# Performance work log

Hardware: AMD Instinct MI355X
Metric: run time of the kernel (lower is better)

The kernel has to match this reference:

```python
import jax, jax.numpy as jnp
import numpy as np

N_NODES = 50000
N_EDGES = 800000
NUM_FEATURES = 128
HIDDEN = 128
NUM_CLASSES = 10
NUM_GRAPHS = 512
PROCESSING_STEPS = 4


def setup_inputs() -> dict:
    key = jax.random.key(0)
    ks = jax.random.split(key, 20)
    s = 0.05
    inp = {
        'x': jax.random.normal(ks[0], (N_NODES, NUM_FEATURES), jnp.float32),
        'edge_index': jax.random.randint(ks[1], (2, N_EDGES), 0, N_NODES),
        'batch': jnp.sort(jax.random.randint(ks[2], (N_NODES,), 0, NUM_GRAPHS)),
        # GCN layers (weights stored [in, out])
        'W1': jax.random.normal(ks[3], (NUM_FEATURES, HIDDEN), jnp.float32) * s,
        'b1': jnp.zeros((HIDDEN,), jnp.float32),
        'W2': jax.random.normal(ks[4], (HIDDEN, HIDDEN), jnp.float32) * s,
        'b2': jnp.zeros((HIDDEN,), jnp.float32),
        'W3': jax.random.normal(ks[5], (HIDDEN, HIDDEN), jnp.float32) * s,
        'b3': jnp.zeros((HIDDEN,), jnp.float32),
        # Set2Set LSTM cell: input 2*HIDDEN -> hidden HIDDEN, torch gate order i,f,g,o
        'Wih': jax.random.normal(ks[6], (4 * HIDDEN, 2 * HIDDEN), jnp.float32) * s,
        'Whh': jax.random.normal(ks[7], (4 * HIDDEN, HIDDEN), jnp.float32) * s,
        'bih': jnp.zeros((4 * HIDDEN,), jnp.float32),
        'bhh': jnp.zeros((4 * HIDDEN,), jnp.float32),
        # MLP head
        'L1w': jax.random.normal(ks[8], (2 * HIDDEN, HIDDEN), jnp.float32) * s,
        'L1b': jnp.zeros((HIDDEN,), jnp.float32),
        'L2w': jax.random.normal(ks[9], (HIDDEN, HIDDEN // 2), jnp.float32) * s,
        'L2b': jnp.zeros((HIDDEN // 2,), jnp.float32),
        'L3w': jax.random.normal(ks[10], (HIDDEN // 2, NUM_CLASSES), jnp.float32) * s,
        'L3b': jnp.zeros((NUM_CLASSES,), jnp.float32),
    }
    return inp


def _gcn_conv(x, row, col, W, b, n):
    # PyG GCNConv: x @ W, symmetric normalization with self-loops, scatter-add to targets.
    xw = x @ W  # [N, out]
    deg = jax.ops.segment_sum(jnp.ones_like(col, dtype=xw.dtype), col, num_segments=n)
    dis = jnp.where(deg > 0, jax.lax.rsqrt(jnp.maximum(deg, 1.0)), 0.0)
    norm = dis[row] * dis[col]  # [E+N]
    out = jax.ops.segment_sum(norm[:, None] * xw[row], col, num_segments=n)
    return out + b


def _segment_softmax(e, batch, n_seg):
    emax = jax.lax.stop_gradient(jax.ops.segment_max(e, batch, num_segments=n_seg))
    emax = jnp.where(jnp.isfinite(emax), emax, 0.0)
    a = jnp.exp(e - emax[batch])
    asum = jax.ops.segment_sum(a, batch, num_segments=n_seg)
    return a / jnp.where(asum > 0, asum, 1.0)[batch]


def reference(x, edge_index, batch, W1, b1, W2, b2, W3, b3,
              Wih, Whh, bih, bhh, L1w, L1b, L2w, L2b, L3w, L3b):
    n = x.shape[0]
    # add self loops once
    loops = jnp.arange(n, dtype=edge_index.dtype)
    row = jnp.concatenate([edge_index[0], loops])  # sources
    col = jnp.concatenate([edge_index[1], loops])  # targets

    h = jax.nn.relu(_gcn_conv(x, row, col, W1, b1, n))
    h = jax.nn.relu(_gcn_conv(h, row, col, W2, b2, n))
    h = jax.nn.relu(_gcn_conv(h, row, col, W3, b3, n))

    # Set2Set readout (processing_steps=4)
    d = h.shape[1]
    hs = jnp.zeros((NUM_GRAPHS, d), h.dtype)
    cs = jnp.zeros((NUM_GRAPHS, d), h.dtype)
    q_star = jnp.zeros((NUM_GRAPHS, 2 * d), h.dtype)
    for _ in range(PROCESSING_STEPS):
        gates = q_star @ Wih.T + hs @ Whh.T + bih + bhh  # [B, 4d]
        ig, fg, gg, og = jnp.split(gates, 4, axis=-1)
        cs = jax.nn.sigmoid(fg) * cs + jax.nn.sigmoid(ig) * jnp.tanh(gg)
        q = jax.nn.sigmoid(og) * jnp.tanh(cs)
        hs = q
        e = jnp.sum(h * q[batch], axis=-1)  # [N]
        a = _segment_softmax(e, batch, NUM_GRAPHS)
        r = jax.ops.segment_sum(a[:, None] * h, batch, num_segments=NUM_GRAPHS)
        q_star = jnp.concatenate([q, r], axis=-1)

    # MLP head (dropout inactive in eval)
    y = jax.nn.relu(q_star @ L1w + L1b)
    y = jax.nn.relu(y @ L2w + L2b)
    y = y @ L3w + L3b
    return jax.nn.log_softmax(y, axis=-1)
```

## Files before the change

### kernel.cpp

```cpp
#include <hip/hip_runtime.h>

constexpr int NN  = 50000;
constexpr int NE  = 800000;
constexpr int FD  = 128;
constexpr int NG  = 512;
constexpr int NB  = 4;
constexpr int BCAP = 24;
constexpr int CAP = NB * BCAP;
constexpr int SLICE = 12500;

typedef __attribute__((ext_vector_type(8))) short bf16x8;
typedef __attribute__((ext_vector_type(4))) float f32x4;

__device__ __forceinline__ float bf2f(unsigned short u) {
    unsigned int v = ((unsigned int)u) << 16;
    float f; __builtin_memcpy(&f, &v, 4); return f;
}
__device__ __forceinline__ unsigned short f2bf(float f) {
    unsigned int u; __builtin_memcpy(&u, &f, 4);
    u += 0x7FFFu + ((u >> 16) & 1u);
    return (unsigned short)(u >> 16);
}
__device__ __forceinline__ float2 bfp(unsigned int u) {
    unsigned int lo = u << 16, hi = u & 0xFFFF0000u;
    float2 r; __builtin_memcpy(&r.x, &lo, 4); __builtin_memcpy(&r.y, &hi, 4);
    return r;
}
__device__ __forceinline__ unsigned int packbf(float a, float b) {
    return (unsigned int)f2bf(a) | ((unsigned int)f2bf(b) << 16);
}
__device__ __forceinline__ float sigmoidf(float x) { return 1.0f / (1.0f + __expf(-x)); }
__device__ __forceinline__ float ldw(const void* p, int idx, int flag) {
    return flag ? ((const float*)p)[idx] : bf2f(((const unsigned short*)p)[idx]);
}

__global__ void k_detect(const unsigned int* __restrict__ xw, int* __restrict__ flag,
                         int* __restrict__ bcnt) {
    int gid = blockIdx.x * 256 + threadIdx.x;
    if (gid < NN * NB) bcnt[gid] = 0;
    if (blockIdx.x == 0) {
        __shared__ int cnt;
        if (threadIdx.x == 0) cnt = 0;
        __syncthreads();
        int local = 0;
        for (int i = threadIdx.x; i < 2048; i += 256) {
            unsigned int w = xw[i];
            unsigned int h0 = w & 0xFFFFu, h1 = w >> 16;
            if (((h0 >> 7) & 0xFF) >= 0x90) local++;
            if (((h1 >> 7) & 0xFF) >= 0x90) local++;
        }
        atomicAdd(&cnt, local);
        __syncthreads();
        if (threadIdx.x == 0) *flag = (cnt > 256) ? 1 : 0;
    }
}

__global__ void k_cvt_x(const void* __restrict__ src, unsigned short* __restrict__ dst,
                        const int* __restrict__ batch, int* __restrict__ goff,
                        const int* __restrict__ flagp) {
    int i = blockIdx.x * 256 + threadIdx.x;
    if (i < NN * FD) {
        if (*flagp) dst[i] = f2bf(((const float*)src)[i]);
        else        dst[i] = ((const unsigned short*)src)[i];
    }
    if (i < NN) {
        int b = batch[i];
        if (b < 0) b = 0;
        if (b >= NG) b = NG - 1;
        int prev;
        if (i == 0) prev = -1;
        else {
            prev = batch[i - 1];
            if (prev < 0) prev = 0;
            if (prev >= NG) prev = NG - 1;
        }
        for (int g = prev + 1; g <= b; g++) goff[g] = i;
        if (i == NN - 1)
            for (int g = b + 1; g <= NG; g++) goff[g] = NN;
    }
}

struct WDesc {
    const void* src[16];
    unsigned short* dst[16];
    int off[17];
};
__global__ void k_cvt_w(WDesc d, const int* __restrict__ flagp) {
    int gid = blockIdx.x * 256 + threadIdx.x;
    if (gid >= d.off[16]) return;
    int t = 0;
    while (gid >= d.off[t + 1]) t++;
    int i = gid - d.off[t];
    if (*flagp) d.dst[t][i] = f2bf(((const float*)d.src[t])[i]);
    else        d.dst[t][i] = ((const unsigned short*)d.src[t])[i];
}

__global__ void k_wt(const void* __restrict__ Wih, const void* __restrict__ Whh,
                     const void* __restrict__ bih, const void* __restrict__ bhh,
                     unsigned int* __restrict__ WcombT,
                     unsigned int* __restrict__ WrT,
                     float* __restrict__ bsum, const int* __restrict__ flagp) {
    int gid = blockIdx.x * 256 + threadIdx.x;
    int flag = *flagp;
    if (gid < 64 * 512) {
        int k2 = gid >> 9, row = gid & 511;
        float a0 = ldw(Wih, row * 256 + 2 * k2, flag)     + ldw(Whh, row * 128 + 2 * k2, flag);
        float a1 = ldw(Wih, row * 256 + 2 * k2 + 1, flag) + ldw(Whh, row * 128 + 2 * k2 + 1, flag);
        WcombT[gid] = packbf(a0, a1);
    } else if (gid < 2 * 64 * 512) {
        int g2 = gid - 64 * 512;
        int k2 = g2 >> 9, row = g2 & 511;
        WrT[g2] = packbf(ldw(Wih, row * 256 + 128 + 2 * k2, flag),
                         ldw(Wih, row * 256 + 128 + 2 * k2 + 1, flag));
    } else if (gid < 2 * 64 * 512 + 512) {
        int row = gid - 2 * 64 * 512;
        bsum[row] = ldw(bih, row, flag) + ldw(bhh, row, flag);
    }
}

__global__ void k_fill(const int* __restrict__ ei, int* __restrict__ bcnt,
                       unsigned short* __restrict__ csr_row) {
    int e = blockIdx.x * 256 + threadIdx.x;
    if (e < NE) {
        int r = ei[e], c = ei[NE + e];
        if ((unsigned)r >= (unsigned)NN) r = 0;
        if ((unsigned)c >= (unsigned)NN) c = 0;
        int b = r / SLICE;
        int pos = atomicAdd(&bcnt[c * NB + b], 1);
        if (pos < BCAP) csr_row[c * CAP + b * BCAP + pos] = (unsigned short)r;
    }
}

__global__ __launch_bounds__(256) void k_gemm(const unsigned short* __restrict__ H,
                                              const unsigned short* __restrict__ W,
                                              const int4* __restrict__ bcnt4,
                                              unsigned short* __restrict__ XW, int M) {
    __shared__ unsigned short WB[128 * 136];
    int t = threadIdx.x;
    unsigned int* WBu = (unsigned int*)WB;
    for (int idx = t; idx < 128 * 64; idx += 256) {
        int n = idx & 127, k2 = idx >> 7;
        unsigned int u0 = W[(2 * k2) * 128 + n];
        unsigned int u1 = W[(2 * k2 + 1) * 128 + n];
        WBu[n * 68 + k2] = u0 | (u1 << 16);
    }
    __syncthreads();
    int wave = t >> 6, lane = t & 63;
    int lm = lane & 15;
    int lq = lane >> 4;
    int row = blockIdx.x * 64 + wave * 16 + lm;
    int rowc = (row < M) ? row : (M - 1);
    const unsigned short* Arow = H + (size_t)rowc * 128;
    f32x4 acc[8];
#pragma unroll
    for (int n = 0; n < 8; n++) acc[n] = (f32x4){0.f, 0.f, 0.f, 0.f};
#pragma unroll
    for (int kk = 0; kk < 4; kk++) {
        bf16x8 afrag = *(const bf16x8*)(Arow + kk * 32 + lq * 8);
        const unsigned short* wbase = WB + kk * 32 + lq * 8;
#pragma unroll
        for (int n = 0; n < 8; n++) {
            bf16x8 bfrag = *(const bf16x8*)(wbase + (n * 16 + lm) * 136);
            acc[n] = __builtin_amdgcn_mfma_f32_16x16x32_bf16(afrag, bfrag, acc[n], 0, 0, 0);
        }
    }
    int rbase = blockIdx.x * 64 + wave * 16 + lq * 4;
#pragma unroll
    for (int r = 0; r < 4; r++) {
        int orow = rbase + r;
        if (orow < M) {
            int4 bc = bcnt4[orow];
            float dn = rsqrtf((float)(bc.x + bc.y + bc.z + bc.w + 1));
            unsigned short* orow_p = XW + (size_t)orow * 128 + lm;
#pragma unroll
            for (int n = 0; n < 8; n++) orow_p[n * 16] = f2bf(acc[n][r] * dn);
        }
    }
}

__global__ __launch_bounds__(256) void k_aggr(const unsigned short* __restrict__ XW,
                                              const int4* __restrict__ bcnt4,
                                              const unsigned short* __restrict__ csr_row,
                                              const unsigned short* __restrict__ bias,
                                              unsigned short* __restrict__ Hout) {
    int wave = threadIdx.x >> 6;
    int lane = threadIdx.x & 63;
    int nsel = lane >> 4;
    int sub  = lane & 15;
    int node = blockIdx.x * 16 + wave * 4 + nsel;
    if (node >= NN) return;
    const uint4* XW4 = (const uint4*)XW;
    int4 bc = bcnt4[node];
    int deg = bc.x + bc.y + bc.z + bc.w;
    float dn = rsqrtf((float)(deg + 1));
    uint4 sv = XW4[(size_t)node * 16 + sub];
    float2 s0 = bfp(sv.x), s1 = bfp(sv.y), s2 = bfp(sv.z), s3 = bfp(sv.w);
    float a0 = s0.x, a1 = s0.y, a2 = s1.x, a3 = s1.y;
    float a4 = s2.x, a5 = s2.y, a6 = s3.x, a7 = s3.y;
    int cnts[NB] = {bc.x, bc.y, bc.z, bc.w};
    const unsigned short* lst = csr_row + node * CAP;
#pragma unroll
    for (int b = 0; b < NB; b++) {
        int n = cnts[b]; if (n > BCAP) n = BCAP;
        const unsigned short* lb = lst + b * BCAP;
        int j = 0;
        for (; j + 4 <= n; j += 4) {
            int r0 = lb[j], r1 = lb[j + 1], r2 = lb[j + 2], r3 = lb[j + 3];
            uint4 v0 = XW4[(size_t)r0 * 16 + sub];
            uint4 v1 = XW4[(size_t)r1 * 16 + sub];
            uint4 v2 = XW4[(size_t)r2 * 16 + sub];
            uint4 v3 = XW4[(size_t)r3 * 16 + sub];
            float2 f;
            f = bfp(v0.x); a0 += f.x; a1 += f.y;
            f = bfp(v0.y); a2 += f.x; a3 += f.y;
            f = bfp(v0.z); a4 += f.x; a5 += f.y;
            f = bfp(v0.w); a6 += f.x; a7 += f.y;
            f = bfp(v1.x); a0 += f.x; a1 += f.y;
            f = bfp(v1.y); a2 += f.x; a3 += f.y;
            f = bfp(v1.z); a4 += f.x; a5 += f.y;
            f = bfp(v1.w); a6 += f.x; a7 += f.y;
            f = bfp(v2.x); a0 += f.x; a1 += f.y;
            f = bfp(v2.y); a2 += f.x; a3 += f.y;
            f = bfp(v2.z); a4 += f.x; a5 += f.y;
            f = bfp(v2.w); a6 += f.x; a7 += f.y;
            f = bfp(v3.x); a0 += f.x; a1 += f.y;
            f = bfp(v3.y); a2 += f.x; a3 += f.y;
            f = bfp(v3.z); a4 += f.x; a5 += f.y;
            f = bfp(v3.w); a6 += f.x; a7 += f.y;
        }
        for (; j < n; j++) {
            int r = lb[j];
            uint4 v = XW4[(size_t)r * 16 + sub];
            float2 f;
            f = bfp(v.x); a0 += f.x; a1 += f.y;
            f = bfp(v.y); a2 += f.x; a3 += f.y;
            f = bfp(v.z); a4 += f.x; a5 += f.y;
            f = bfp(v.w); a6 += f.x; a7 += f.y;
        }
    }
    uint4 bv = ((const uint4*)bias)[sub];
    float2 b0 = bfp(bv.x), b1 = bfp(bv.y), b2 = bfp(bv.z), b3 = bfp(bv.w);
    uint4 o;
    o.x = packbf(fmaxf(dn * a0 + b0.x, 0.0f), fmaxf(dn * a1 + b0.y, 0.0f));
    o.y = packbf(fmaxf(dn * a2 + b1.x, 0.0f), fmaxf(dn * a3 + b1.y, 0.0f));
    o.z = packbf(fmaxf(dn * a4 + b2.x, 0.0f), fmaxf(dn * a5 + b2.y, 0.0f));
    o.w = packbf(fmaxf(dn * a6 + b3.x, 0.0f), fmaxf(dn * a7 + b3.y, 0.0f));
    ((uint4*)Hout)[(size_t)node * 16 + sub] = o;
}

__global__ __launch_bounds__(512) void k_s2s(const unsigned short* __restrict__ H,
                                             const int* __restrict__ goff,
                                             const unsigned int* __restrict__ WcombT,
                                             const unsigned int* __restrict__ WrT,
                                             const float* __restrict__ bsum,
                                             const unsigned short* __restrict__ L1w,
                                             const unsigned short* __restrict__ L1b,
                                             const unsigned short* __restrict__ L2w,
                                             const unsigned short* __restrict__ L2b,
                                             const unsigned short* __restrict__ L3w,
                                             const unsigned short* __restrict__ L3b,
                                             void* __restrict__ out,
                                             const int* __restrict__ flagp) {
    int g = blockIdx.x, t = threadIdx.x;
    __shared__ float qsr[256];
    __shared__ float hsv[128], csv[128];
    __shared__ float gates[512];
    __shared__ float wred[8];
    __shared__ float wrr[8][128];
    __shared__ float ps[128];
    __shared__ float qrep[4 * 132];
    __shared__ float y1[128], y2[64], y3[10], lseS[1];

    if (t < 256) qsr[t] = 0.0f;
    if (t < 128) { hsv[t] = 0.0f; csv[t] = 0.0f; }
    __syncthreads();

    int s = goff[g], e = goff[g + 1];
    if (s < 0) s = 0;
    if (e > NN) e = NN;
    if (e < s) e = s;
    int w = t >> 6, lane = t & 63;
    const unsigned int* Hu = (const unsigned int*)H;

    int nq = t >> 2;
    int fq = (t & 3) * 16;
    const float* qc = qrep + (t & 3) * 132 + 2 * fq;

    for (int step = 0; step < 4; step++) {
        {
            float acc = bsum[t];
#pragma unroll 8
            for (int k2 = 0; k2 < 64; k2++) {
                float2 wv = bfp(WcombT[k2 * 512 + t]);
                acc += wv.x * hsv[2 * k2] + wv.y * hsv[2 * k2 + 1];
            }
#pragma unroll 8
            for (int k2 = 0; k2 < 64; k2++) {
                float2 wv = bfp(WrT[k2 * 512 + t]);
                acc += wv.x * qsr[128 + 2 * k2] + wv.y * qsr[128 + 2 * k2 + 1];
            }
            gates[t] = acc;
        }
        __syncthreads();
        if (t < 128) {
            float ig = sigmoidf(gates[t]),       fg = sigmoidf(gates[128 + t]);
            float gg = tanhf(gates[256 + t]),    og = sigmoidf(gates[384 + t]);
            float c = fg * csv[t] + ig * gg;
            float q = og * tanhf(c);
            csv[t] = c;
            hsv[t] = q;
            qsr[t] = q;
            qrep[t] = q; qrep[132 + t] = q; qrep[264 + t] = q; qrep[396 + t] = q;
        }
        __syncthreads();

        float m = -1e30f, l = 0.0f, r0 = 0.0f, r1 = 0.0f;
        for (int cs = s; cs < e; cs += 128) {
            int ce = cs + 128; if (ce > e) ce = e;
            int nid = cs + nq;
            float eacc = 0.0f;
            if (nid < ce) {
                const unsigned int* hrow = Hu + (size_t)nid * 64 + fq;
#pragma unroll
                for (int u = 0; u < 16; u += 4) {
                    uint4 hv = *(const uint4*)(hrow + u);
                    float2 f0 = bfp(hv.x), f1 = bfp(hv.y);
                    float2 f2 = bfp(hv.z), f3 = bfp(hv.w);
                    const float* qp = qc + 2 * u;
                    eacc += f0.x * qp[0] + f0.y * qp[1] + f1.x * qp[2] + f1.y * qp[3]
                          + f2.x * qp[4] + f2.y * qp[5] + f3.x * qp[6] + f3.y * qp[7];
                }
            }
            eacc += __shfl_xor(eacc, 1);
            eacc += __shfl_xor(eacc, 2);
            float esc = (nid < ce) ? eacc : -1e30f;
            float vmax = esc;
            for (int d = 4; d < 64; d <<= 1) vmax = fmaxf(vmax, __shfl_xor(vmax, d));
            if (lane == 0) wred[w] = vmax;
            __syncthreads();
            float M = m;
#pragma unroll
            for (int k = 0; k < 8; k++) M = fmaxf(M, wred[k]);
            float p = __expf(esc - M);
            bool lead = ((t & 3) == 0) && (nid < ce);
            if (lead) ps[nq] = p;
            float psum = lead ? p : 0.0f;
            for (int d = 1; d < 64; d <<= 1) psum += __shfl_xor(psum, d);
            __syncthreads();
            if (lane == 0) wred[w] = psum;
            __syncthreads();
            float Lc = 0.0f;
#pragma unroll
            for (int k = 0; k < 8; k++) Lc += wred[k];
            float scale = __expf(m - M);
            l = l * scale + Lc;
            r0 *= scale; r1 *= scale;
            m = M;
            int i = cs + w;
            for (; i + 24 < ce; i += 32) {
                float p0 = ps[i - cs],      p1 = ps[i + 8 - cs];
                float p2 = ps[i + 16 - cs], p3 = ps[i + 24 - cs];
                unsigned int v0 = Hu[(size_t)i * 64 + lane];
                unsigned int v1 = Hu[(size_t)(i + 8) * 64 + lane];
                unsigned int v2 = Hu[(size_t)(i + 16) * 64 + lane];
                unsigned int v3 = Hu[(size_t)(i + 24) * 64 + lane];
                float2 f0 = bfp(v0), f1 = bfp(v1), f2 = bfp(v2), f3 = bfp(v3);
                r0 += p0 * f0.x + p1 * f1.x + p2 * f2.x + p3 * f3.x;
                r1 += p0 * f0.y + p1 * f1.y + p2 * f2.y + p3 * f3.y;
            }
            for (; i < ce; i += 8) {
                float p0 = ps[i - cs];
                float2 f = bfp(Hu[(size_t)i * 64 + lane]);
                r0 += p0 * f.x; r1 += p0 * f.y;
            }
            __syncthreads();
        }
        wrr[w][2 * lane]     = r0;
        wrr[w][2 * lane + 1] = r1;
        __syncthreads();
        if (t < 128) {
            float R = 0.0f;
#pragma unroll
            for (int k = 0; k < 8; k++) R += wrr[k][t];
            float L = l;
            if (!(L > 0.0f)) L = 1.0f;
            qsr[128 + t] = R / L;
        }
        __syncthreads();
    }

    if (t < 128) {
        float acc = bf2f(L1b[t]);
        for (int i = 0; i < 256; i++) acc += bf2f(L1w[i * 128 + t]) * qsr[i];
        y1[t] = fmaxf(acc, 0.0f);
    }
    __syncthreads();
    if (t < 64) {
        float a2 = bf2f(L2b[t]);
        for (int i = 0; i < 128; i++) a2 += bf2f(L2w[i * 64 + t]) * y1[i];
        y2[t] = fmaxf(a2, 0.0f);
    }
    __syncthreads();
    if (t < 10) {
        float a3 = bf2f(L3b[t]);
        for (int i = 0; i < 64; i++) a3 += bf2f(L3w[i * 10 + t]) * y2[i];
        y3[t] = a3;
    }
    __syncthreads();
    if (t == 0) {
        float m = y3[0];
        for (int i = 1; i < 10; i++) m = fmaxf(m, y3[i]);
        float s2 = 0.0f;
        for (int i = 0; i < 10; i++) s2 += __expf(y3[i] - m);
        lseS[0] = m + __logf(s2);
    }
    __syncthreads();
    if (t < 10) {
        float v = y3[t] - lseS[0];
        if (!(v == v)) v = -9.0f;
        if (*flagp) ((float*)out)[g * 10 + t] = v;
        else        ((unsigned short*)out)[g * 10 + t] = f2bf(v);
    }
}

extern "C" void kernel_launch(void* const* d_in, const int* in_sizes, int n_in,
                              void* d_out, int out_size, void* d_ws, size_t ws_size,
                              hipStream_t stream) {
    const int* ei  = (const int*)d_in[1];
    const int* bat = (const int*)d_in[2];

    char* base = (char*)d_ws;
    size_t woff = 0;
    auto alloc = [&](size_t bytes) -> void* {
        void* r = base + woff;
        woff = (woff + bytes + 255) & ~(size_t)255;
        return r;
    };
    unsigned short* A = (unsigned short*)alloc((size_t)NN * FD * 2);
    unsigned short* B = (unsigned short*)alloc((size_t)NN * FD * 2);
    unsigned short* csr_row = (unsigned short*)alloc((size_t)NN * CAP * 2);
    int*   bcnt     = (int*)alloc(NN * NB * 4);
    int*   goff     = (int*)alloc((NG + 1) * 4);
    int*   flag     = (int*)alloc(256);
    unsigned int* WcombT = (unsigned int*)alloc(64 * 512 * 4);
    unsigned int* WrT    = (unsigned int*)alloc(64 * 512 * 4);
    float* bsum          = (float*)alloc(512 * 4);
    auto walloc = [&](int n) { return (unsigned short*)alloc((size_t)n * 2); };
    unsigned short* cW1  = walloc(128 * 128);
    unsigned short* cb1  = walloc(128);
    unsigned short* cW2  = walloc(128 * 128);
    unsigned short* cb2  = walloc(128);
    unsigned short* cW3  = walloc(128 * 128);
    unsigned short* cb3  = walloc(128);
    unsigned short* cL1w = walloc(256 * 128);
    unsigned short* cL1b = walloc(128);
    unsigned short* cL2w = walloc(128 * 64);
    unsigned short* cL2b = walloc(64);
    unsigned short* cL3w = walloc(64 * 10);
    unsigned short* cL3b = walloc(10);
    (void)ws_size; (void)in_sizes; (void)n_in; (void)out_size;

    const int nblkZ = (NN * NB + 255) / 256;
    const int nblkE = (NE + 255) / 256;

    k_detect<<<nblkZ, 256, 0, stream>>>((const unsigned int*)d_in[0], flag, bcnt);
    k_cvt_x<<<(NN * FD + 255) / 256, 256, 0, stream>>>(d_in[0], B, bat, goff, flag);
    {
        WDesc d;
        const int idxs[12] = {3,4,5,6,7,8,13,14,15,16,17,18};
        unsigned short* dsts[12] = {cW1,cb1,cW2,cb2,cW3,cb3,
                                    cL1w,cL1b,cL2w,cL2b,cL3w,cL3b};
        const int ns[12] = {128*128,128,128*128,128,128*128,128,
                            256*128,128,128*64,64,64*10,10};
        int acc = 0;
        for (int i = 0; i < 12; i++) {
            d.src[i] = d_in[idxs[i]];
            d.dst[i] = dsts[i];
            d.off[i] = acc;
            acc += ns[i];
        }
        for (int i = 12; i <= 16; i++) d.off[i] = acc;
        k_cvt_w<<<(acc + 255) / 256, 256, 0, stream>>>(d, flag);
    }
    k_wt<<<(2 * 64 * 512 + 512 + 255) / 256, 256, 0, stream>>>(
        d_in[9], d_in[10], d_in[11], d_in[12], WcombT, WrT, bsum, flag);

    k_fill<<<nblkE, 256, 0, stream>>>(ei, bcnt, csr_row);

    const int gemmBlk = (NN + 63) / 64;
    const int aggrBlk = (NN + 15) / 16;

    k_gemm<<<gemmBlk, 256, 0, stream>>>(B, cW1, (const int4*)bcnt, A, NN);
    k_aggr<<<aggrBlk, 256, 0, stream>>>(A, (const int4*)bcnt, csr_row, cb1, B);
    k_gemm<<<gemmBlk, 256, 0, stream>>>(B, cW2, (const int4*)bcnt, A, NN);
    k_aggr<<<aggrBlk, 256, 0, stream>>>(A, (const int4*)bcnt, csr_row, cb2, B);
    k_gemm<<<gemmBlk, 256, 0, stream>>>(B, cW3, (const int4*)bcnt, A, NN);
    k_aggr<<<aggrBlk, 256, 0, stream>>>(A, (const int4*)bcnt, csr_row, cb3, B);

    k_s2s<<<NG, 512, 0, stream>>>(B, goff, WcombT, WrT, bsum,
                                  cL1w, cL1b, cL2w, cL2b, cL3w, cL3b,
                                  d_out, flag);
}
```

Measured before the change: 359.4 us.

## Fuse preprocessing kernels, pre-transpose GEMM weights, stage GEMM output through LDS

Merges detect, x conversion, weight conversion and LSTM weight prep into one preprocessing kernel, which removes three launches. GCN weights are now pre-packed transposed into k-pairs, so each GEMM block loads them into LDS with 16-byte vector copies instead of strided gathers. GEMM output is staged through LDS for coalesced 16-byte row stores. The LSTM gate matvec uses a uint2-interleaved weight layout with four independent accumulators. Every preprocessing block now redundantly runs the dtype-detection scan.

```diff
diff --git a/kernel.cpp b/kernel.cpp
--- a/kernel.cpp
+++ b/kernel.cpp
@@ -34,14 +34,25 @@
     return flag ? ((const float*)p)[idx] : bf2f(((const unsigned short*)p)[idx]);
 }
 
-__global__ void k_detect(const unsigned int* __restrict__ xw, int* __restrict__ flag,
-                         int* __restrict__ bcnt) {
-    int gid = blockIdx.x * 256 + threadIdx.x;
-    if (gid < NN * NB) bcnt[gid] = 0;
-    if (blockIdx.x == 0) {
-        __shared__ int cnt;
-        if (threadIdx.x == 0) cnt = 0;
-        __syncthreads();
+struct PreDesc {
+    const void* src[12];
+    void* dst[12];
+    int kind[12];
+    int off[13];
+};
+__global__ __launch_bounds__(256) void k_pre(const void* __restrict__ xsrc,
+                      unsigned short* __restrict__ xdst,
+                      const int* __restrict__ batch, int* __restrict__ goff,
+                      int* __restrict__ bcnt, int* __restrict__ flagp,
+                      const void* __restrict__ Wih, const void* __restrict__ Whh,
+                      const void* __restrict__ bih, const void* __restrict__ bhh,
+                      unsigned int* __restrict__ WcombT, unsigned int* __restrict__ WrT,
+                      float* __restrict__ bsum, PreDesc d) {
+    __shared__ int cnt;
+    if (threadIdx.x == 0) cnt = 0;
+    __syncthreads();
+    {
+        const unsigned int* xw = (const unsigned int*)xsrc;
         int local = 0;
         for (int i = threadIdx.x; i < 2048; i += 256) {
             unsigned int w = xw[i];
@@ -50,71 +61,58 @@
             if (((h1 >> 7) & 0xFF) >= 0x90) local++;
         }
         atomicAdd(&cnt, local);
-        __syncthreads();
-        if (threadIdx.x == 0) *flag = (cnt > 256) ? 1 : 0;
-    }
-}
-
-__global__ void k_cvt_x(const void* __restrict__ src, unsigned short* __restrict__ dst,
-                        const int* __restrict__ batch, int* __restrict__ goff,
-                        const int* __restrict__ flagp) {
-    int i = blockIdx.x * 256 + threadIdx.x;
-    if (i < NN * FD) {
-        if (*flagp) dst[i] = f2bf(((const float*)src)[i]);
-        else        dst[i] = ((const unsigned short*)src)[i];
-    }
-    if (i < NN) {
-        int b = batch[i];
+    }
+    __syncthreads();
+    int flag = (cnt > 256) ? 1 : 0;
+    int gid = blockIdx.x * 256 + threadIdx.x;
+    if (gid == 0) *flagp = flag;
+    if (gid < NN * NB) bcnt[gid] = 0;
+    if (gid < NN * FD) {
+        if (flag) xdst[gid] = f2bf(((const float*)xsrc)[gid]);
+        else      xdst[gid] = ((const unsigned short*)xsrc)[gid];
+    }
+    if (gid < NN) {
+        int b = batch[gid];
         if (b < 0) b = 0;
         if (b >= NG) b = NG - 1;
         int prev;
-        if (i == 0) prev = -1;
+        if (gid == 0) prev = -1;
         else {
-            prev = batch[i - 1];
+            prev = batch[gid - 1];
             if (prev < 0) prev = 0;
             if (prev >= NG) prev = NG - 1;
         }
-        for (int g = prev + 1; g <= b; g++) goff[g] = i;
-        if (i == NN - 1)
+        for (int g = prev + 1; g <= b; g++) goff[g] = gid;
+        if (gid == NN - 1)
             for (int g = b + 1; g <= NG; g++) goff[g] = NN;
     }
-}
-
-struct WDesc {
-    const void* src[16];
-    unsigned short* dst[16];
-    int off[17];
-};
-__global__ void k_cvt_w(WDesc d, const int* __restrict__ flagp) {
-    int gid = blockIdx.x * 256 + threadIdx.x;
-    if (gid >= d.off[16]) return;
-    int t = 0;
-    while (gid >= d.off[t + 1]) t++;
-    int i = gid - d.off[t];
-    if (*flagp) d.dst[t][i] = f2bf(((const float*)d.src[t])[i]);
-    else        d.dst[t][i] = ((const unsigned short*)d.src[t])[i];
-}
-
-__global__ void k_wt(const void* __restrict__ Wih, const void* __restrict__ Whh,
-                     const void* __restrict__ bih, const void* __restrict__ bhh,
-                     unsigned int* __restrict__ WcombT,
-                     unsigned int* __restrict__ WrT,
-                     float* __restrict__ bsum, const int* __restrict__ flagp) {
-    int gid = blockIdx.x * 256 + threadIdx.x;
-    int flag = *flagp;
     if (gid < 64 * 512) {
         int k2 = gid >> 9, row = gid & 511;
         float a0 = ldw(Wih, row * 256 + 2 * k2, flag)     + ldw(Whh, row * 128 + 2 * k2, flag);
         float a1 = ldw(Wih, row * 256 + 2 * k2 + 1, flag) + ldw(Whh, row * 128 + 2 * k2 + 1, flag);
-        WcombT[gid] = packbf(a0, a1);
+        WcombT[(k2 >> 1) * 1024 + 2 * row + (k2 & 1)] = packbf(a0, a1);
     } else if (gid < 2 * 64 * 512) {
         int g2 = gid - 64 * 512;
         int k2 = g2 >> 9, row = g2 & 511;
-        WrT[g2] = packbf(ldw(Wih, row * 256 + 128 + 2 * k2, flag),
-                         ldw(Wih, row * 256 + 128 + 2 * k2 + 1, flag));
+        WrT[(k2 >> 1) * 1024 + 2 * row + (k2 & 1)] =
+            packbf(ldw(Wih, row * 256 + 128 + 2 * k2, flag),
+                   ldw(Wih, row * 256 + 128 + 2 * k2 + 1, flag));
     } else if (gid < 2 * 64 * 512 + 512) {
         int row = gid - 2 * 64 * 512;
         bsum[row] = ldw(bih, row, flag) + ldw(bhh, row, flag);
+    }
+    if (gid < d.off[12]) {
+        int t = 0;
+        while (gid >= d.off[t + 1]) t++;
+        int i = gid - d.off[t];
+        if (d.kind[t] == 0) {
+            if (flag) ((unsigned short*)d.dst[t])[i] = f2bf(((const float*)d.src[t])[i]);
+            else      ((unsigned short*)d.dst[t])[i] = ((const unsigned short*)d.src[t])[i];
+        } else {
+            int n = i >> 6, k2 = i & 63;
+            ((unsigned int*)d.dst[t])[i] = packbf(ldw(d.src[t], (2 * k2) * 128 + n, flag),
+                                                  ldw(d.src[t], (2 * k2 + 1) * 128 + n, flag));
+        }
     }
 }
 
@@ -132,17 +130,16 @@
 }
 
 __global__ __launch_bounds__(256) void k_gemm(const unsigned short* __restrict__ H,
-                                              const unsigned short* __restrict__ W,
+                                              const unsigned int* __restrict__ WT,
                                               const int4* __restrict__ bcnt4,
                                               unsigned short* __restrict__ XW, int M) {
-    __shared__ unsigned short WB[128 * 136];
+    __shared__ alignas(16) unsigned short WB[128 * 136];
     int t = threadIdx.x;
     unsigned int* WBu = (unsigned int*)WB;
-    for (int idx = t; idx < 128 * 64; idx += 256) {
-        int n = idx & 127, k2 = idx >> 7;
-        unsigned int u0 = W[(2 * k2) * 128 + n];
-        unsigned int u1 = W[(2 * k2 + 1) * 128 + n];
-        WBu[n * 68 + k2] = u0 | (u1 << 16);
+    for (int c = t; c < 2048; c += 256) {
+        uint4 v = ((const uint4*)WT)[c];
+        int n = c >> 4, k2q = c & 15;
+        *(uint4*)(WBu + n * 68 + k2q * 4) = v;
     }
     __syncthreads();
     int wave = t >> 6, lane = t & 63;
@@ -164,17 +161,25 @@
             acc[n] = __builtin_amdgcn_mfma_f32_16x16x32_bf16(afrag, bfrag, acc[n], 0, 0, 0);
         }
     }
-    int rbase = blockIdx.x * 64 + wave * 16 + lq * 4;
+    __syncthreads();
 #pragma unroll
     for (int r = 0; r < 4; r++) {
-        int orow = rbase + r;
-        if (orow < M) {
-            int4 bc = bcnt4[orow];
-            float dn = rsqrtf((float)(bc.x + bc.y + bc.z + bc.w + 1));
-            unsigned short* orow_p = XW + (size_t)orow * 128 + lm;
-#pragma unroll
-            for (int n = 0; n < 8; n++) orow_p[n * 16] = f2bf(acc[n][r] * dn);
-        }
+        int row_local = wave * 16 + lq * 4 + r;
+        int orow = blockIdx.x * 64 + row_local;
+        int oc = (orow < M) ? orow : (M - 1);
+        int4 bc = bcnt4[oc];
+        float dn = rsqrtf((float)(bc.x + bc.y + bc.z + bc.w + 1));
+#pragma unroll
+        for (int n = 0; n < 8; n++)
+            WB[row_local * 136 + n * 16 + lm] = f2bf(acc[n][r] * dn);
+    }
+#pragma unroll
+    for (int it = 0; it < 4; it++) {
+        int row_local = wave * 16 + it * 4 + (lane >> 4);
+        int row_global = blockIdx.x * 64 + row_local;
+        uint4 v = *(const uint4*)(WB + row_local * 136 + (lane & 15) * 8);
+        if (row_global < M)
+            *((uint4*)(XW + (size_t)row_global * 128) + (lane & 15)) = v;
     }
 }
 
@@ -285,21 +290,27 @@
     int nq = t >> 2;
     int fq = (t & 3) * 16;
     const float* qc = qrep + (t & 3) * 132 + 2 * fq;
+    const uint2* WC2 = (const uint2*)WcombT;
+    const uint2* WR2 = (const uint2*)WrT;
 
     for (int step = 0; step < 4; step++) {
         {
-            float acc = bsum[t];
+            float accA = bsum[t], accB = 0.0f, accC = 0.0f, accD = 0.0f;
 #pragma unroll 8
-            for (int k2 = 0; k2 < 64; k2++) {
-                float2 wv = bfp(WcombT[k2 * 512 + t]);
-                acc += wv.x * hsv[2 * k2] + wv.y * hsv[2 * k2 + 1];
+            for (int p = 0; p < 32; p++) {
+                uint2 u = WC2[p * 512 + t];
+                float2 w0 = bfp(u.x), w1 = bfp(u.y);
+                accA += w0.x * hsv[4 * p];     accB += w0.y * hsv[4 * p + 1];
+                accC += w1.x * hsv[4 * p + 2]; accD += w1.y * hsv[4 * p + 3];
             }
 #pragma unroll 8
-            for (int k2 = 0; k2 < 64; k2++) {
-                float2 wv = bfp(WrT[k2 * 512 + t]);
-                acc += wv.x * qsr[128 + 2 * k2] + wv.y * qsr[128 + 2 * k2 + 1];
+            for (int p = 0; p < 32; p++) {
+                uint2 u = WR2[p * 512 + t];
+                float2 w0 = bfp(u.x), w1 = bfp(u.y);
+                accA += w0.x * qsr[128 + 4 * p];     accB += w0.y * qsr[128 + 4 * p + 1];
+                accC += w1.x * qsr[128 + 4 * p + 2]; accD += w1.y * qsr[128 + 4 * p + 3];
             }
-            gates[t] = acc;
+            gates[t] = (accA + accB) + (accC + accD);
         }
         __syncthreads();
         if (t < 128) {
@@ -445,12 +456,12 @@
     unsigned int* WcombT = (unsigned int*)alloc(64 * 512 * 4);
     unsigned int* WrT    = (unsigned int*)alloc(64 * 512 * 4);
     float* bsum          = (float*)alloc(512 * 4);
+    unsigned int* cWT1 = (unsigned int*)alloc(8192 * 4);
+    unsigned int* cWT2 = (unsigned int*)alloc(8192 * 4);
+    unsigned int* cWT3 = (unsigned int*)alloc(8192 * 4);
     auto walloc = [&](int n) { return (unsigned short*)alloc((size_t)n * 2); };
-    unsigned short* cW1  = walloc(128 * 128);
     unsigned short* cb1  = walloc(128);
-    unsigned short* cW2  = walloc(128 * 128);
     unsigned short* cb2  = walloc(128);
-    unsigned short* cW3  = walloc(128 * 128);
     unsigned short* cb3  = walloc(128);
     unsigned short* cL1w = walloc(256 * 128);
     unsigned short* cL1b = walloc(128);
@@ -460,41 +471,40 @@
     unsigned short* cL3b = walloc(10);
     (void)ws_size; (void)in_sizes; (void)n_in; (void)out_size;
 
-    const int nblkZ = (NN * NB + 255) / 256;
-    const int nblkE = (NE + 255) / 256;
-
-    k_detect<<<nblkZ, 256, 0, stream>>>((const unsigned int*)d_in[0], flag, bcnt);
-    k_cvt_x<<<(NN * FD + 255) / 256, 256, 0, stream>>>(d_in[0], B, bat, goff, flag);
     {
-        WDesc d;
-        const int idxs[12] = {3,4,5,6,7,8,13,14,15,16,17,18};
-        unsigned short* dsts[12] = {cW1,cb1,cW2,cb2,cW3,cb3,
-                                    cL1w,cL1b,cL2w,cL2b,cL3w,cL3b};
-        const int ns[12] = {128*128,128,128*128,128,128*128,128,
-                            256*128,128,128*64,64,64*10,10};
+        PreDesc d;
+        const int idxs[12]  = {3,    4,  5,    6,  7,    8,  13, 14, 15, 16, 17, 18};
+        void* dsts[12]      = {cWT1, cb1, cWT2, cb2, cWT3, cb3,
+                               cL1w, cL1b, cL2w, cL2b, cL3w, cL3b};
+        const int kinds[12] = {1, 0, 1, 0, 1, 0, 0, 0, 0, 0, 0, 0};
+        const int ns[12]    = {8192, 128, 8192, 128, 8192, 128,
+                               256 * 128, 128, 128 * 64, 64, 64 * 10, 10};
         int acc = 0;
         for (int i = 0; i < 12; i++) {
             d.src[i] = d_in[idxs[i]];
             d.dst[i] = dsts[i];
+            d.kind[i] = kinds[i];
             d.off[i] = acc;
             acc += ns[i];
         }
-        for (int i = 12; i <= 16; i++) d.off[i] = acc;
-        k_cvt_w<<<(acc + 255) / 256, 256, 0, stream>>>(d, flag);
-    }
-    k_wt<<<(2 * 64 * 512 + 512 + 255) / 256, 256, 0, stream>>>(
-        d_in[9], d_in[10], d_in[11], d_in[12], WcombT, WrT, bsum, flag);
-
+        d.off[12] = acc;
+        const int nblkPre = (NN * FD + 255) / 256;
+        k_pre<<<nblkPre, 256, 0, stream>>>(d_in[0], B, bat, goff, bcnt, flag,
+                                           d_in[9], d_in[10], d_in[11], d_in[12],
+                                           WcombT, WrT, bsum, d);
+    }
+
+    const int nblkE = (NE + 255) / 256;
     k_fill<<<nblkE, 256, 0, stream>>>(ei, bcnt, csr_row);
 
     const int gemmBlk = (NN + 63) / 64;
     const int aggrBlk = (NN + 15) / 16;
 
-    k_gemm<<<gemmBlk, 256, 0, stream>>>(B, cW1, (const int4*)bcnt, A, NN);
+    k_gemm<<<gemmBlk, 256, 0, stream>>>(B, cWT1, (const int4*)bcnt, A, NN);
     k_aggr<<<aggrBlk, 256, 0, stream>>>(A, (const int4*)bcnt, csr_row, cb1, B);
-    k_gemm<<<gemmBlk, 256, 0, stream>>>(B, cW2, (const int4*)bcnt, A, NN);
+    k_gemm<<<gemmBlk, 256, 0, stream>>>(B, cWT2, (const int4*)bcnt, A, NN);
     k_aggr<<<aggrBlk, 256, 0, stream>>>(A, (const int4*)bcnt, csr_row, cb2, B);
-    k_gemm<<<gemmBlk, 256, 0, stream>>>(B, cW3, (const int4*)bcnt, A, NN);
+    k_gemm<<<gemmBlk, 256, 0, stream>>>(B, cWT3, (const int4*)bcnt, A, NN);
     k_aggr<<<aggrBlk, 256, 0, stream>>>(A, (const int4*)bcnt, csr_row, cb3, B);
 
     k_s2s<<<NG, 512, 0, stream>>>(B, goff, WcombT, WrT, bsum,
```

New measurement: 401.0 us. +11.6%, slower.
